# Kernel optimization log

Hardware: AMD Instinct MI355X
Metric: run time of the kernel (lower is better)

## Reference

```python
import jax, jax.numpy as jnp
import numpy as np

B, T, C, H = 2, 4096, 512, 8
HD = C // H  # head_dim = 64


def setup_inputs() -> dict:
    key = jax.random.key(0)
    ks = jax.random.split(key, 5)
    s = 0.02
    return {
        "x": jax.random.normal(ks[0], (B, T, C), dtype=jnp.float32),
        "Wqkv": jax.random.normal(ks[1], (C, 3 * C), dtype=jnp.float32) * s,
        "bqkv": jax.random.normal(ks[2], (3 * C,), dtype=jnp.float32) * s,
        "Wproj": jax.random.normal(ks[3], (C, C), dtype=jnp.float32) * s,
        "bproj": jax.random.normal(ks[4], (C,), dtype=jnp.float32) * s,
    }


def reference(x, Wqkv, bqkv, Wproj, bproj):
    b, t, c = x.shape
    qkv = x @ Wqkv + bqkv                      # [B,T,3C]
    q, k, v = jnp.split(qkv, 3, axis=-1)
    # [B,T,C] -> [B,H,T,HD]
    q = q.reshape(b, t, H, HD).transpose(0, 2, 1, 3)
    k = k.reshape(b, t, H, HD).transpose(0, 2, 1, 3)
    v = v.reshape(b, t, H, HD).transpose(0, 2, 1, 3)
    att = jnp.einsum("bhqd,bhkd->bhqk", q, k) / jnp.sqrt(jnp.float32(HD))
    causal = jnp.tril(jnp.ones((t, t), dtype=bool))
    att = jnp.where(causal, att, -jnp.inf)
    att = jax.nn.softmax(att, axis=-1)
    y = jnp.einsum("bhqk,bhkd->bhqd", att, v)  # [B,H,T,HD]
    y = y.transpose(0, 2, 1, 3).reshape(b, t, c)
    return y @ Wproj + bproj
```

## Files before the change

kernel.cpp:

```cpp
#include <hip/hip_runtime.h>
#include <math.h>

#define NB 2
#define NT 4096
#define NC 512
#define NH 8
#define ND 64
#define N3C (3*NC)

typedef __attribute__((ext_vector_type(8))) __bf16 bf16x8;
typedef __attribute__((ext_vector_type(4))) __bf16 bf16x4;
typedef __attribute__((ext_vector_type(4))) float  f32x4;

__device__ __forceinline__ void load_lds16(const __bf16* g, __bf16* l) {
    __builtin_amdgcn_global_load_lds(
        (const __attribute__((address_space(1))) void*)g,
        (__attribute__((address_space(3))) void*)l, 16, 0, 0);
}

__global__ __launch_bounds__(256) void cvt_bf16_kernel(
    const float* __restrict__ x, __bf16* __restrict__ xb, int n)
{
    const int i = (blockIdx.x * 256 + threadIdx.x) << 3;
    if (i < n) {
        float4 a = *(const float4*)(x + i);
        float4 b = *(const float4*)(x + i + 4);
        bf16x8 o;
        o[0] = (__bf16)a.x; o[1] = (__bf16)a.y; o[2] = (__bf16)a.z; o[3] = (__bf16)a.w;
        o[4] = (__bf16)b.x; o[5] = (__bf16)b.y; o[6] = (__bf16)b.z; o[7] = (__bf16)b.w;
        *(bf16x8*)(xb + i) = o;
    }
}

__global__ __launch_bounds__(256) void prep_kernel(
    const float* __restrict__ Wqkv, const float* __restrict__ Wproj,
    __bf16* __restrict__ wqkvt, __bf16* __restrict__ wprojt)
{
    __shared__ float T[64][65];
    int id = blockIdx.x;
    const float* W; __bf16* Wt; int N, n0, k0;
    if (id < 192) { W = Wqkv;  Wt = wqkvt;  N = N3C; n0 = (id % 24) << 6; k0 = (id / 24) << 6; }
    else { id -= 192; W = Wproj; Wt = wprojt; N = NC;  n0 = (id & 7) << 6;  k0 = (id >> 3) << 6; }
    const int K = NC;

    const int tx = threadIdx.x & 15, ty = threadIdx.x >> 4;
#pragma unroll
    for (int i = 0; i < 4; ++i) {
        const int r = ty + (i << 4);
        float4 v = *(const float4*)(W + (size_t)(k0 + r) * N + n0 + (tx << 2));
        T[r][(tx << 2) + 0] = v.x;
        T[r][(tx << 2) + 1] = v.y;
        T[r][(tx << 2) + 2] = v.z;
        T[r][(tx << 2) + 3] = v.w;
    }
    __syncthreads();
#pragma unroll
    for (int i = 0; i < 4; ++i) {
        const int nr = ty + (i << 4);
        bf16x4 o;
        o[0] = (__bf16)T[(tx << 2) + 0][nr];
        o[1] = (__bf16)T[(tx << 2) + 1][nr];
        o[2] = (__bf16)T[(tx << 2) + 2][nr];
        o[3] = (__bf16)T[(tx << 2) + 3][nr];
        *(bf16x4*)(Wt + (size_t)(n0 + nr) * K + k0 + (tx << 2)) = o;
    }
}

template<int BM>
__global__ __launch_bounds__(256) void gemm_glds_kernel(
    const __bf16* __restrict__ A, const __bf16* __restrict__ Bt,
    const float* __restrict__ bias, void* __restrict__ Cout,
    int M, int N, int K, int out_bf16)
{
    constexpr int IT = BM / 32;
    constexpr int AI = BM / 32;
    __shared__ __align__(16) __bf16 As[BM * 64];
    __shared__ __align__(16) __bf16 Bs[128 * 64];

    const int tid  = threadIdx.x;
    const int w    = tid >> 6, lane = tid & 63;
    const int g    = lane >> 4, n = lane & 15;
    const int n7   = n & 7;
    const int wr   = (w >> 1) * (BM / 2);
    const int wc   = (w & 1) << 6;
    const int m0   = blockIdx.y * BM, n0 = blockIdx.x << 7;

    const __bf16* ag[AI]; __bf16* al[AI];
#pragma unroll
    for (int q = 0; q < AI; ++q) {
        const int G = w * (BM * 2) + q * 64 + lane;
        const int r = G >> 3, pg = G & 7, kg = pg ^ (r & 7);
        ag[q] = A + (size_t)(m0 + r) * K + (kg << 3);
        al[q] = As + ((w * (BM * 2) + q * 64) << 3);
    }
    const __bf16* bg[4]; __bf16* bl[4];
#pragma unroll
    for (int q = 0; q < 4; ++q) {
        const int G = w * 256 + q * 64 + lane;
        const int r = G >> 3, pg = G & 7, kg = pg ^ (r & 7);
        bg[q] = Bt + (size_t)(n0 + r) * K + (kg << 3);
        bl[q] = Bs + ((w * 256 + q * 64) << 3);
    }

    f32x4 acc[IT][4];
#pragma unroll
    for (int i = 0; i < IT; ++i)
#pragma unroll
        for (int j = 0; j < 4; ++j) acc[i][j] = (f32x4){0.f, 0.f, 0.f, 0.f};

    const int ksteps = K >> 6;
    for (int ks = 0; ks < ksteps; ++ks) {
        __syncthreads();
        const int ko = ks << 6;
#pragma unroll
        for (int q = 0; q < AI; ++q) load_lds16(ag[q] + ko, al[q]);
#pragma unroll
        for (int q = 0; q < 4;  ++q) load_lds16(bg[q] + ko, bl[q]);
        __syncthreads();

#pragma unroll
        for (int s = 0; s < 2; ++s) {
            bf16x8 af[IT], bf[4];
#pragma unroll
            for (int i = 0; i < IT; ++i) {
                const int row = wr + (i << 4) + n;
                af[i] = *(const bf16x8*)&As[(row << 6) + ((((s << 2) + g) ^ n7) << 3)];
            }
#pragma unroll
            for (int j = 0; j < 4; ++j) {
                const int row = wc + (j << 4) + n;
                bf[j] = *(const bf16x8*)&Bs[(row << 6) + ((((s << 2) + g) ^ n7) << 3)];
            }
#pragma unroll
            for (int i = 0; i < IT; ++i)
#pragma unroll
                for (int j = 0; j < 4; ++j)
                    acc[i][j] = __builtin_amdgcn_mfma_f32_16x16x32_bf16(af[i], bf[j], acc[i][j], 0, 0, 0);
        }
    }

#pragma unroll
    for (int j = 0; j < 4; ++j) {
        const int colg = n0 + wc + (j << 4) + n;
        const float bb = bias[colg];
#pragma unroll
        for (int i = 0; i < IT; ++i) {
#pragma unroll
            for (int reg = 0; reg < 4; ++reg) {
                const int rowg = m0 + wr + (i << 4) + (g << 2) + reg;
                const float v = acc[i][j][reg] + bb;
                if (out_bf16)
                    ((__bf16*)Cout)[(size_t)rowg * N + colg] = (__bf16)v;
                else
                    ((float*)Cout)[(size_t)rowg * N + colg] = v;
            }
        }
    }
}

__global__ __launch_bounds__(512) void attn_kernel(
    const __bf16* __restrict__ qkv, int mono, __bf16* __restrict__ outb,
    float* __restrict__ Opart, float* __restrict__ Lpart)
{
    __shared__ __align__(16) unsigned char SMEM[36864];
    __bf16 (*QPs)[72] = (__bf16(*)[72])SMEM;
    __bf16 (*Ks)[72]  = (__bf16(*)[72])(SMEM + 18432);
    __bf16 (*Vt)[72]  = (__bf16(*)[72])(SMEM + 27648);

    const int tid  = threadIdx.x;
    const int xi   = blockIdx.x;
    const int bh   = blockIdx.y;
    const int b    = bh >> 3, h = bh & 7;

    int qb, jt0, jt1, pid;
    if (mono) {
        qb = (bh < 8) ? (31 - xi) : xi;
        jt0 = 0; jt1 = (qb << 1) + 2; pid = 0;
    } else {
        const int a  = (xi < 8) ? 0 : ((xi < 24) ? 1 : ((xi < 48) ? 2 : 3));
        const int np = a + 1;
        const int off = xi - 4 * a * np;
        qb = (a << 3) + off / np;
        const int p  = off % np;
        const int ntiles = (qb << 1) + 2;
        const int chunk = ntiles / np, rem = ntiles % np;
        jt0 = p * chunk + (p < rem ? p : rem);
        jt1 = jt0 + chunk + (p < rem ? 1 : 0);
        pid = bh * 80 + xi;
    }

    const int qr0  = qb << 7;
    const size_t base = (size_t)b * NT * N3C;
    const int col  = h * ND;

    const int w    = tid >> 6;
    const int lane = tid & 63;
    const int g    = lane >> 4;
    const int n    = lane & 15;
    const int qg   = w >> 1;
    const int kh   = w & 1;
    const int qrow0 = qg << 5;
    const int kcol0 = kh << 5;
    const int sw   = (g ^ (n >> 2)) << 3;

    const int kr = tid >> 3;
    const int kc = (tid & 7) << 3;
    const int vd = lane;
    const int vk = w << 2;

    const __bf16* kptr = qkv + base + NC + col + kc;
    const __bf16* vptr = qkv + base + 2 * NC + col + vd;

#pragma unroll
    for (int i = 0; i < 2; ++i) {
        const int r = kr + (i << 6);
        bf16x8 v = *(const bf16x8*)(qkv + base + (size_t)(qr0 + r) * N3C + col + kc);
        bf16x8 q;
#pragma unroll
        for (int j = 0; j < 8; ++j) q[j] = (__bf16)(0.125f * (float)v[j]);
        *(bf16x8*)&QPs[r][kc] = q;
    }
    __syncthreads();

    bf16x8 qf[2][2];
#pragma unroll
    for (int qt = 0; qt < 2; ++qt)
#pragma unroll
        for (int hh = 0; hh < 2; ++hh)
            qf[qt][hh] = *(const bf16x8*)&QPs[qrow0 + (qt << 4) + n][(hh << 5) + (g << 3)];

    bf16x8 ones;
#pragma unroll
    for (int j = 0; j < 8; ++j) ones[j] = (__bf16)1.0f;

    f32x4 O[2][4];
#pragma unroll
    for (int qt = 0; qt < 2; ++qt)
#pragma unroll
        for (int dt = 0; dt < 4; ++dt) O[qt][dt] = (f32x4){0.f, 0.f, 0.f, 0.f};
    f32x4 L[2] = {{0.f,0.f,0.f,0.f},{0.f,0.f,0.f,0.f}};

    const int r0 = jt0 << 6;
    bf16x8 kreg = *(const bf16x8*)(kptr + (size_t)(r0 + kr) * N3C);
    __bf16 vreg[8];
#pragma unroll
    for (int j = 0; j < 4; ++j) {
        vreg[j]     = vptr[(size_t)(r0 + vk + j) * N3C];
        vreg[4 + j] = vptr[(size_t)(r0 + vk + 32 + j) * N3C];
    }

    for (int jt = jt0; jt < jt1; ++jt) {
        __syncthreads();
        *(bf16x8*)&Ks[kr][kc] = kreg;
        {
            bf16x4 va, vb;
#pragma unroll
            for (int j = 0; j < 4; ++j) { va[j] = vreg[j]; vb[j] = vreg[4 + j]; }
            *(bf16x4*)&Vt[vd][vk]      = va;
            *(bf16x4*)&Vt[vd][vk + 32] = vb;
        }
        __syncthreads();

        if (jt + 1 < jt1) {
            const int kr1 = (jt + 1) << 6;
            kreg = *(const bf16x8*)(kptr + (size_t)(kr1 + kr) * N3C);
#pragma unroll
            for (int j = 0; j < 4; ++j) {
                vreg[j]     = vptr[(size_t)(kr1 + vk + j) * N3C];
                vreg[4 + j] = vptr[(size_t)(kr1 + vk + 32 + j) * N3C];
            }
        }

        f32x4 S[2][2];
        __builtin_amdgcn_s_setprio(1);
#pragma unroll
        for (int t = 0; t < 2; ++t) {
            const bf16x8 k0 = *(const bf16x8*)&Ks[kcol0 + (t << 4) + n][(g << 3)];
            const bf16x8 k1 = *(const bf16x8*)&Ks[kcol0 + (t << 4) + n][32 + (g << 3)];
#pragma unroll
            for (int qt = 0; qt < 2; ++qt) {
                f32x4 a = {0.f, 0.f, 0.f, 0.f};
                a = __builtin_amdgcn_mfma_f32_16x16x32_bf16(qf[qt][0], k0, a, 0, 0, 0);
                a = __builtin_amdgcn_mfma_f32_16x16x32_bf16(qf[qt][1], k1, a, 0, 0, 0);
                S[qt][t] = a;
            }
        }
        __builtin_amdgcn_s_setprio(0);

        if (jt >= (qb << 1)) {
#pragma unroll
            for (int qt = 0; qt < 2; ++qt)
#pragma unroll
                for (int t = 0; t < 2; ++t)
#pragma unroll
                    for (int reg = 0; reg < 4; ++reg) {
                        const int kg = (jt << 6) + kcol0 + (t << 4) + n;
                        const int qgl = qr0 + qrow0 + (qt << 4) + (g << 2) + reg;
                        if (kg > qgl) S[qt][t][reg] = -INFINITY;
                    }
        }

#pragma unroll
        for (int qt = 0; qt < 2; ++qt)
#pragma unroll
            for (int t = 0; t < 2; ++t)
#pragma unroll
                for (int reg = 0; reg < 4; ++reg)
                    QPs[qrow0 + (qt << 4) + (g << 2) + reg]
                       [kcol0 + (((t << 4) + n) ^ (g << 3))] =
                        (__bf16)__expf(S[qt][t][reg]);

        bf16x8 vf[4];
#pragma unroll
        for (int dt = 0; dt < 4; ++dt) {
            const int vr = (dt << 4) + n;
            vf[dt] = *(const bf16x8*)&Vt[vr][kcol0 + (g << 3)];
        }

        __builtin_amdgcn_s_setprio(1);
#pragma unroll
        for (int qt = 0; qt < 2; ++qt) {
            const bf16x8 p = *(const bf16x8*)&QPs[qrow0 + (qt << 4) + n][kcol0 + sw];
            L[qt] = __builtin_amdgcn_mfma_f32_16x16x32_bf16(p, ones, L[qt], 0, 0, 0);
#pragma unroll
            for (int dt = 0; dt < 4; ++dt)
                O[qt][dt] = __builtin_amdgcn_mfma_f32_16x16x32_bf16(p, vf[dt], O[qt][dt], 0, 0, 0);
        }
        __builtin_amdgcn_s_setprio(0);
    }

    __syncthreads();
    float* red = (float*)SMEM;
    if (kh == 1) {
#pragma unroll
        for (int qt = 0; qt < 2; ++qt)
#pragma unroll
            for (int reg = 0; reg < 4; ++reg) {
                const int qlx = qrow0 + (qt << 4) + (g << 2) + reg;
#pragma unroll
                for (int dt = 0; dt < 4; ++dt)
                    red[qlx * 64 + (dt << 4) + n] = O[qt][dt][reg];
                if (n == 0) red[8192 + qlx] = L[qt][reg];
            }
    }
    __syncthreads();
    if (kh == 0) {
#pragma unroll
        for (int qt = 0; qt < 2; ++qt)
#pragma unroll
            for (int reg = 0; reg < 4; ++reg) {
                const int qlx = qrow0 + (qt << 4) + (g << 2) + reg;
                const float Ltot = L[qt][reg] + red[8192 + qlx];
                if (mono) {
                    const float inv = 1.0f / Ltot;
                    const size_t row = (size_t)b * NT + qr0 + qlx;
#pragma unroll
                    for (int dt = 0; dt < 4; ++dt)
                        outb[row * NC + col + (dt << 4) + n] =
                            (__bf16)((O[qt][dt][reg] + red[qlx * 64 + (dt << 4) + n]) * inv);
                } else {
                    if (n == 0) Lpart[(size_t)pid * 128 + qlx] = Ltot;
#pragma unroll
                    for (int dt = 0; dt < 4; ++dt)
                        Opart[(size_t)pid * 8192 + qlx * 64 + (dt << 4) + n] =
                            O[qt][dt][reg] + red[qlx * 64 + (dt << 4) + n];
                }
            }
    }
}

__global__ __launch_bounds__(256) void combine_kernel(
    const float* __restrict__ Opart, const float* __restrict__ Lpart,
    __bf16* __restrict__ outb)
{
    const int gid = blockIdx.x;
    const int qb  = gid & 31, bh = gid >> 5;
    const int b   = bh >> 3, h = bh & 7;
    const int a   = qb >> 3, r7 = qb & 7;
    const int np  = a + 1;
    const int pbase = bh * 80 + 4 * a * np + r7 * np;

    const int tid = threadIdx.x;
    const int c   = (tid & 15) << 2;
    const int rb  = tid >> 4;
#pragma unroll
    for (int pass = 0; pass < 8; ++pass) {
        const int r = rb + (pass << 4);
        float Ls = 0.f;
        f32x4 acc = {0.f, 0.f, 0.f, 0.f};
        for (int p = 0; p < np; ++p) {
            Ls += Lpart[(size_t)(pbase + p) * 128 + r];
            const f32x4 v = *(const f32x4*)&Opart[(size_t)(pbase + p) * 8192 + (r << 6) + c];
            acc += v;
        }
        const float inv = 1.0f / Ls;
        bf16x4 o;
        o[0] = (__bf16)(acc[0] * inv); o[1] = (__bf16)(acc[1] * inv);
        o[2] = (__bf16)(acc[2] * inv); o[3] = (__bf16)(acc[3] * inv);
        *(bf16x4*)&outb[((size_t)b * NT + (qb << 7) + r) * NC + h * ND + c] = o;
    }
}

extern "C" void kernel_launch(void* const* d_in, const int* in_sizes, int n_in,
                              void* d_out, int out_size, void* d_ws, size_t ws_size,
                              hipStream_t stream)
{
    const float* x     = (const float*)d_in[0];
    const float* Wqkv  = (const float*)d_in[1];
    const float* bqkv  = (const float*)d_in[2];
    const float* Wproj = (const float*)d_in[3];
    const float* bproj = (const float*)d_in[4];
    float* out = (float*)d_out;

    char* ws = (char*)d_ws;
    __bf16* xb     = (__bf16*)(ws);
    __bf16* qkvb   = (__bf16*)(ws + 8388608);
    __bf16* attb   = (__bf16*)(ws + 33554432);
    __bf16* wqkvt  = (__bf16*)(ws + 41943040);
    __bf16* wprojt = (__bf16*)(ws + 43515904);
    float*  Opart  = (float*)(ws + 44040192);
    float*  Lpart  = (float*)(ws + 85983232);
    const size_t SPLIT_NEED = 86638592;

    cvt_bf16_kernel<<<dim3(2048), dim3(256), 0, stream>>>(x, xb, NB * NT * NC);
    prep_kernel<<<dim3(256), dim3(256), 0, stream>>>(Wqkv, Wproj, wqkvt, wprojt);

    gemm_glds_kernel<128><<<dim3(N3C / 128, (NB * NT) / 128), dim3(256), 0, stream>>>(
        xb, wqkvt, bqkv, qkvb, NB * NT, N3C, NC, 1);

    if (ws_size >= SPLIT_NEED) {
        attn_kernel<<<dim3(80, NB * NH), dim3(512), 0, stream>>>(
            qkvb, 0, attb, Opart, Lpart);
        combine_kernel<<<dim3(512), dim3(256), 0, stream>>>(Opart, Lpart, attb);
    } else {
        attn_kernel<<<dim3(NT / 128, NB * NH), dim3(512), 0, stream>>>(
            qkvb, 1, attb, (float*)nullptr, (float*)nullptr);
    }

    gemm_glds_kernel<64><<<dim3(NC / 128, (NB * NT) / 64), dim3(256), 0, stream>>>(
        attb, wprojt, bproj, out, NB * NT, NC, NC, 0);
}
```

Measured before the change: 204.0 us.

## Shrink attention query tile to 64 rows with 256-thread blocks and finer split

Halves the attention query block from 128 to 64 rows and runs each block with 4 waves instead of 8. It doubles the number of split-K partitions to 160 per head, and the combine kernel is resized to match. Each thread now loads twice the K/V data per tile, and LDS use shrinks so more blocks can be resident per CU. The aim is better load balance and occupancy across the causal triangle. The cost is more blocks, so Q and K/V are reloaded more often, and there are more partial outputs to write and combine.

```diff
diff --git a/kernel.cpp b/kernel.cpp
--- a/kernel.cpp
+++ b/kernel.cpp
@@ -158,38 +158,38 @@
     }
 }
 
-__global__ __launch_bounds__(512) void attn_kernel(
+__global__ __launch_bounds__(256, 4) void attn_kernel(
     const __bf16* __restrict__ qkv, int mono, __bf16* __restrict__ outb,
     float* __restrict__ Opart, float* __restrict__ Lpart)
 {
-    __shared__ __align__(16) unsigned char SMEM[36864];
+    __shared__ __align__(16) unsigned char SMEM[27648];
     __bf16 (*QPs)[72] = (__bf16(*)[72])SMEM;
-    __bf16 (*Ks)[72]  = (__bf16(*)[72])(SMEM + 18432);
-    __bf16 (*Vt)[72]  = (__bf16(*)[72])(SMEM + 27648);
+    __bf16 (*Ks)[72]  = (__bf16(*)[72])(SMEM + 9216);
+    __bf16 (*Vt)[72]  = (__bf16(*)[72])(SMEM + 18432);
 
     const int tid  = threadIdx.x;
     const int xi   = blockIdx.x;
     const int bh   = blockIdx.y;
     const int b    = bh >> 3, h = bh & 7;
 
-    int qb, jt0, jt1, pid;
+    int m, jt0, jt1, pid;
     if (mono) {
-        qb = (bh < 8) ? (31 - xi) : xi;
-        jt0 = 0; jt1 = (qb << 1) + 2; pid = 0;
+        m = (bh < 8) ? (63 - xi) : xi;
+        jt0 = 0; jt1 = m + 1; pid = 0;
     } else {
-        const int a  = (xi < 8) ? 0 : ((xi < 24) ? 1 : ((xi < 48) ? 2 : 3));
+        const int a  = (xi < 16) ? 0 : ((xi < 48) ? 1 : ((xi < 96) ? 2 : 3));
         const int np = a + 1;
-        const int off = xi - 4 * a * np;
-        qb = (a << 3) + off / np;
+        const int off = xi - 8 * a * (a + 1);
+        m = (a << 4) + off / np;
         const int p  = off % np;
-        const int ntiles = (qb << 1) + 2;
-        const int chunk = ntiles / np, rem = ntiles % np;
+        const int ntk = m + 1;
+        const int chunk = ntk / np, rem = ntk % np;
         jt0 = p * chunk + (p < rem ? p : rem);
         jt1 = jt0 + chunk + (p < rem ? 1 : 0);
-        pid = bh * 80 + xi;
-    }
-
-    const int qr0  = qb << 7;
+        pid = bh * 160 + xi;
+    }
+
+    const int qr0  = m << 6;
     const size_t base = (size_t)b * NT * N3C;
     const int col  = h * ND;
 
@@ -206,14 +206,14 @@
     const int kr = tid >> 3;
     const int kc = (tid & 7) << 3;
     const int vd = lane;
-    const int vk = w << 2;
+    const int vk = w << 3;
 
     const __bf16* kptr = qkv + base + NC + col + kc;
     const __bf16* vptr = qkv + base + 2 * NC + col + vd;
 
 #pragma unroll
     for (int i = 0; i < 2; ++i) {
-        const int r = kr + (i << 6);
+        const int r = kr + (i << 5);
         bf16x8 v = *(const bf16x8*)(qkv + base + (size_t)(qr0 + r) * N3C + col + kc);
         bf16x8 q;
 #pragma unroll
@@ -241,33 +241,40 @@
     f32x4 L[2] = {{0.f,0.f,0.f,0.f},{0.f,0.f,0.f,0.f}};
 
     const int r0 = jt0 << 6;
-    bf16x8 kreg = *(const bf16x8*)(kptr + (size_t)(r0 + kr) * N3C);
-    __bf16 vreg[8];
-#pragma unroll
-    for (int j = 0; j < 4; ++j) {
+    bf16x8 kreg[2];
+#pragma unroll
+    for (int i = 0; i < 2; ++i)
+        kreg[i] = *(const bf16x8*)(kptr + (size_t)(r0 + kr + (i << 5)) * N3C);
+    __bf16 vreg[16];
+#pragma unroll
+    for (int j = 0; j < 8; ++j) {
         vreg[j]     = vptr[(size_t)(r0 + vk + j) * N3C];
-        vreg[4 + j] = vptr[(size_t)(r0 + vk + 32 + j) * N3C];
+        vreg[8 + j] = vptr[(size_t)(r0 + vk + 32 + j) * N3C];
     }
 
     for (int jt = jt0; jt < jt1; ++jt) {
         __syncthreads();
-        *(bf16x8*)&Ks[kr][kc] = kreg;
+#pragma unroll
+        for (int i = 0; i < 2; ++i)
+            *(bf16x8*)&Ks[kr + (i << 5)][kc] = kreg[i];
         {
-            bf16x4 va, vb;
-#pragma unroll
-            for (int j = 0; j < 4; ++j) { va[j] = vreg[j]; vb[j] = vreg[4 + j]; }
-            *(bf16x4*)&Vt[vd][vk]      = va;
-            *(bf16x4*)&Vt[vd][vk + 32] = vb;
+            bf16x8 va, vb;
+#pragma unroll
+            for (int j = 0; j < 8; ++j) { va[j] = vreg[j]; vb[j] = vreg[8 + j]; }
+            *(bf16x8*)&Vt[vd][vk]      = va;
+            *(bf16x8*)&Vt[vd][vk + 32] = vb;
         }
         __syncthreads();
 
         if (jt + 1 < jt1) {
             const int kr1 = (jt + 1) << 6;
-            kreg = *(const bf16x8*)(kptr + (size_t)(kr1 + kr) * N3C);
-#pragma unroll
-            for (int j = 0; j < 4; ++j) {
+#pragma unroll
+            for (int i = 0; i < 2; ++i)
+                kreg[i] = *(const bf16x8*)(kptr + (size_t)(kr1 + kr + (i << 5)) * N3C);
+#pragma unroll
+            for (int j = 0; j < 8; ++j) {
                 vreg[j]     = vptr[(size_t)(kr1 + vk + j) * N3C];
-                vreg[4 + j] = vptr[(size_t)(kr1 + vk + 32 + j) * N3C];
+                vreg[8 + j] = vptr[(size_t)(kr1 + vk + 32 + j) * N3C];
             }
         }
 
@@ -287,7 +294,7 @@
         }
         __builtin_amdgcn_s_setprio(0);
 
-        if (jt >= (qb << 1)) {
+        if (jt == m) {
 #pragma unroll
             for (int qt = 0; qt < 2; ++qt)
 #pragma unroll
@@ -340,7 +347,7 @@
 #pragma unroll
                 for (int dt = 0; dt < 4; ++dt)
                     red[qlx * 64 + (dt << 4) + n] = O[qt][dt][reg];
-                if (n == 0) red[8192 + qlx] = L[qt][reg];
+                if (n == 0) red[4096 + qlx] = L[qt][reg];
             }
     }
     __syncthreads();
@@ -350,7 +357,7 @@
 #pragma unroll
             for (int reg = 0; reg < 4; ++reg) {
                 const int qlx = qrow0 + (qt << 4) + (g << 2) + reg;
-                const float Ltot = L[qt][reg] + red[8192 + qlx];
+                const float Ltot = L[qt][reg] + red[4096 + qlx];
                 if (mono) {
                     const float inv = 1.0f / Ltot;
                     const size_t row = (size_t)b * NT + qr0 + qlx;
@@ -359,10 +366,10 @@
                         outb[row * NC + col + (dt << 4) + n] =
                             (__bf16)((O[qt][dt][reg] + red[qlx * 64 + (dt << 4) + n]) * inv);
                 } else {
-                    if (n == 0) Lpart[(size_t)pid * 128 + qlx] = Ltot;
+                    if (n == 0) Lpart[(size_t)pid * 64 + qlx] = Ltot;
 #pragma unroll
                     for (int dt = 0; dt < 4; ++dt)
-                        Opart[(size_t)pid * 8192 + qlx * 64 + (dt << 4) + n] =
+                        Opart[(size_t)pid * 4096 + qlx * 64 + (dt << 4) + n] =
                             O[qt][dt][reg] + red[qlx * 64 + (dt << 4) + n];
                 }
             }
@@ -374,30 +381,30 @@
     __bf16* __restrict__ outb)
 {
     const int gid = blockIdx.x;
-    const int qb  = gid & 31, bh = gid >> 5;
+    const int m   = gid & 63, bh = gid >> 6;
     const int b   = bh >> 3, h = bh & 7;
-    const int a   = qb >> 3, r7 = qb & 7;
+    const int a   = m >> 4;
     const int np  = a + 1;
-    const int pbase = bh * 80 + 4 * a * np + r7 * np;
+    const int pbase = bh * 160 + 8 * a * (a + 1) + (m & 15) * np;
 
     const int tid = threadIdx.x;
     const int c   = (tid & 15) << 2;
     const int rb  = tid >> 4;
 #pragma unroll
-    for (int pass = 0; pass < 8; ++pass) {
+    for (int pass = 0; pass < 4; ++pass) {
         const int r = rb + (pass << 4);
         float Ls = 0.f;
         f32x4 acc = {0.f, 0.f, 0.f, 0.f};
         for (int p = 0; p < np; ++p) {
-            Ls += Lpart[(size_t)(pbase + p) * 128 + r];
-            const f32x4 v = *(const f32x4*)&Opart[(size_t)(pbase + p) * 8192 + (r << 6) + c];
+            Ls += Lpart[(size_t)(pbase + p) * 64 + r];
+            const f32x4 v = *(const f32x4*)&Opart[(size_t)(pbase + p) * 4096 + (r << 6) + c];
             acc += v;
         }
         const float inv = 1.0f / Ls;
         bf16x4 o;
         o[0] = (__bf16)(acc[0] * inv); o[1] = (__bf16)(acc[1] * inv);
         o[2] = (__bf16)(acc[2] * inv); o[3] = (__bf16)(acc[3] * inv);
-        *(bf16x4*)&outb[((size_t)b * NT + (qb << 7) + r) * NC + h * ND + c] = o;
+        *(bf16x4*)&outb[((size_t)b * NT + (m << 6) + r) * NC + h * ND + c] = o;
     }
 }
 
@@ -429,11 +436,11 @@
         xb, wqkvt, bqkv, qkvb, NB * NT, N3C, NC, 1);
 
     if (ws_size >= SPLIT_NEED) {
-        attn_kernel<<<dim3(80, NB * NH), dim3(512), 0, stream>>>(
+        attn_kernel<<<dim3(160, NB * NH), dim3(256), 0, stream>>>(
             qkvb, 0, attb, Opart, Lpart);
-        combine_kernel<<<dim3(512), dim3(256), 0, stream>>>(Opart, Lpart, attb);
+        combine_kernel<<<dim3(1024), dim3(256), 0, stream>>>(Opart, Lpart, attb);
     } else {
-        attn_kernel<<<dim3(NT / 128, NB * NH), dim3(512), 0, stream>>>(
+        attn_kernel<<<dim3(64, NB * NH), dim3(256), 0, stream>>>(
             qkvb, 1, attb, (float*)nullptr, (float*)nullptr);
     }
 
```

Result: no change. 206.4 us (+1.2%).
